# Kernel tuning notes

Hardware: AMD Instinct MI355X
Metric: run time of the kernel (lower is better)

The kernel has to match this reference:

```python
import jax, jax.numpy as jnp
import numpy as np

COMMITMENT_COST = 0.25


def setup_inputs() -> dict:
    key = jax.random.key(0)
    k1, k2 = jax.random.split(key)
    x = jax.random.normal(k1, (65536, 256), dtype=jnp.float32)
    codebook = jax.random.normal(k2, (1024, 256), dtype=jnp.float32)
    return {"x": x, "codebook": codebook}


def reference(x, codebook):
    # Flatten to [N, D] (already 2D here).
    flat = x.reshape(-1, codebook.shape[1])
    # Squared euclidean distances [N, K]; argmin matches torch.cdist argmin.
    x2 = jnp.sum(flat * flat, axis=1, keepdims=True)          # [N, 1]
    c2 = jnp.sum(codebook * codebook, axis=1)                  # [K]
    d2 = x2 - 2.0 * (flat @ codebook.T) + c2[None, :]          # [N, K]
    encoding_indices = jnp.argmin(d2, axis=1)                  # [N]
    quantized = codebook[encoding_indices]                     # [N, D]
    # VQ loss + commitment loss
    vq_loss = jnp.mean((jax.lax.stop_gradient(quantized) - flat) ** 2)
    commitment_loss = jnp.mean((quantized - jax.lax.stop_gradient(flat)) ** 2)
    quantization_loss = vq_loss + COMMITMENT_COST * commitment_loss
    # Straight-through estimator
    quantized_st = flat + jax.lax.stop_gradient(quantized - flat)
    quantized_st = quantized_st.reshape(x.shape)
    return quantized_st, quantization_loss, encoding_indices
```

## Files before the change

### kernel.cpp

```cpp
#include <hip/hip_runtime.h>

#define NROWS 65536
#define DDIM  256
#define KCODES 1024
#define MARGIN 0.05f
#define TIE_WINDOW 8.0e-5
#define FLAGCAP 8192

typedef __attribute__((ext_vector_type(8))) short bf16x8;
typedef __attribute__((ext_vector_type(4))) float f32x4;

union F4 { float4 v; float f[4]; };

__device__ __forceinline__ unsigned bf16rne(float f) {
    unsigned u = __float_as_uint(f);
    return (u + 0x7fffu + ((u >> 16) & 1u)) >> 16;
}
__device__ __forceinline__ float bf16tof(unsigned h) {
    return __uint_as_float(h << 16);
}

__global__ __launch_bounds__(64) void c2_kernel(const float* __restrict__ cb,
                                                float* __restrict__ c2f,
                                                double* __restrict__ c2d,
                                                int* __restrict__ cnt) {
    const int c = blockIdx.x, lane = threadIdx.x;
    if (c == 0 && lane == 0) cnt[0] = 0;
    F4 v; v.v = reinterpret_cast<const float4*>(cb + (size_t)c * DDIM)[lane];
    double s = (double)v.f[0] * v.f[0] + (double)v.f[1] * v.f[1]
             + (double)v.f[2] * v.f[2] + (double)v.f[3] * v.f[3];
    #pragma unroll
    for (int off = 32; off; off >>= 1) s += __shfl_xor(s, off);
    if (lane == 0) { c2d[c] = s; c2f[c] = (float)s; }
}

__global__ __launch_bounds__(256) void prep_frags(const float* __restrict__ cb,
                                                  unsigned short* __restrict__ fh,
                                                  unsigned short* __restrict__ fl) {
    int t = blockIdx.x * 256 + threadIdx.x;
    int j0   = (t & 1) * 4;
    int lane = (t >> 1) & 63;
    int ks   = (t >> 7) & 7;
    int ntg  = t >> 10;
    int c = ntg * 16 + (lane & 15);
    int k = ks * 32 + (lane >> 4) * 8 + j0;
    F4 v; v.v = *reinterpret_cast<const float4*>(cb + (size_t)c * DDIM + k);
    unsigned h0 = bf16rne(v.f[0]), h1 = bf16rne(v.f[1]),
             h2 = bf16rne(v.f[2]), h3 = bf16rne(v.f[3]);
    unsigned l0 = bf16rne(v.f[0] - bf16tof(h0)), l1 = bf16rne(v.f[1] - bf16tof(h1)),
             l2 = bf16rne(v.f[2] - bf16tof(h2)), l3 = bf16rne(v.f[3] - bf16tof(h3));
    unsigned* ph = reinterpret_cast<unsigned*>(fh + (size_t)t * 4);
    unsigned* pl = reinterpret_cast<unsigned*>(fl + (size_t)t * 4);
    ph[0] = h0 | (h1 << 16); ph[1] = h2 | (h3 << 16);
    pl[0] = l0 | (l1 << 16); pl[1] = l2 | (l3 << 16);
}

__global__ __launch_bounds__(1024) void vqmfma(const float* __restrict__ x,
                                               const unsigned short* __restrict__ fbh,
                                               const unsigned short* __restrict__ fbl,
                                               const float* __restrict__ c2f,
                                               float* __restrict__ out_idx,
                                               int* __restrict__ flaglist,
                                               int* __restrict__ cnt) {
    __shared__ bf16x8 lds_ah[2048];
    __shared__ bf16x8 lds_al[2048];
    __shared__ float  lds_c2[KCODES];
    __shared__ float  m_b1[512]; __shared__ float m_b2[512]; __shared__ int m_i1[512];

    const int tid  = threadIdx.x;
    const int w    = tid >> 6;
    const int lane = tid & 63;
    const int rh   = w >> 3;
    const int g    = w & 7;
    const int row0 = blockIdx.x * 64;

    lds_c2[tid] = c2f[tid];

    {
        const float4* gx = reinterpret_cast<const float4*>(x + (size_t)row0 * DDIM);
        unsigned* pah = reinterpret_cast<unsigned*>(lds_ah);
        unsigned* pal = reinterpret_cast<unsigned*>(lds_al);
        #pragma unroll
        for (int jj = 0; jj < 4; jj++) {
            int flat4 = jj * 1024 + tid;
            int r = flat4 >> 6;
            int k = (flat4 & 63) * 4;
            F4 v; v.v = gx[flat4];
            int rt = r >> 4, row = r & 15;
            int ks = k >> 5, gg = (k >> 3) & 3, j0 = k & 7;
            int laneS = gg * 16 + row;
            int u32i = ((((rt * 8 + ks) * 64 + laneS) * 8 + j0) >> 1);
            unsigned h0 = bf16rne(v.f[0]), h1 = bf16rne(v.f[1]),
                     h2 = bf16rne(v.f[2]), h3 = bf16rne(v.f[3]);
            pah[u32i]     = h0 | (h1 << 16);
            pah[u32i + 1] = h2 | (h3 << 16);
            unsigned l0 = bf16rne(v.f[0] - bf16tof(h0)), l1 = bf16rne(v.f[1] - bf16tof(h1)),
                     l2 = bf16rne(v.f[2] - bf16tof(h2)), l3 = bf16rne(v.f[3] - bf16tof(h3));
            pal[u32i]     = l0 | (l1 << 16);
            pal[u32i + 1] = l2 | (l3 << 16);
        }
    }
    __syncthreads();

    float bestv[8], secv[8]; int besti[8];
    #pragma unroll
    for (int e = 0; e < 8; e++) { bestv[e] = 1e30f; secv[e] = 1e30f; besti[e] = 0; }

    const bf16x8* Bh = reinterpret_cast<const bf16x8*>(fbh);
    const bf16x8* Bl = reinterpret_cast<const bf16x8*>(fbl);

    for (int cc = 0; cc < KCODES; cc += 256) {
        f32x4 acc[2][2];
        #pragma unroll
        for (int rt = 0; rt < 2; rt++)
            #pragma unroll
            for (int nt = 0; nt < 2; nt++) acc[rt][nt] = (f32x4){0.f, 0.f, 0.f, 0.f};

        const int ntg0 = (cc >> 4) + g * 2;
        const bf16x8* b0h = Bh + (size_t)(ntg0 * 8) * 64 + lane;
        const bf16x8* b0l = Bl + (size_t)(ntg0 * 8) * 64 + lane;
        const bf16x8* b1h = b0h + 8 * 64;
        const bf16x8* b1l = b0l + 8 * 64;
        const bf16x8* a0  = &lds_ah[(rh * 2) * 8 * 64 + lane];
        const bf16x8* a1  = a0 + 8 * 64;
        const bf16x8* a0l = &lds_al[(rh * 2) * 8 * 64 + lane];
        const bf16x8* a1l = a0l + 8 * 64;

        #pragma unroll
        for (int ks = 0; ks < 8; ks++) {
            bf16x8 ah0 = a0[ks * 64],  ah1 = a1[ks * 64];
            bf16x8 al0 = a0l[ks * 64], al1 = a1l[ks * 64];
            bf16x8 bh0 = b0h[ks * 64], bl0 = b0l[ks * 64];
            bf16x8 bh1 = b1h[ks * 64], bl1 = b1l[ks * 64];
            acc[0][0] = __builtin_amdgcn_mfma_f32_16x16x32_bf16(ah0, bh0, acc[0][0], 0, 0, 0);
            acc[1][0] = __builtin_amdgcn_mfma_f32_16x16x32_bf16(ah1, bh0, acc[1][0], 0, 0, 0);
            acc[0][1] = __builtin_amdgcn_mfma_f32_16x16x32_bf16(ah0, bh1, acc[0][1], 0, 0, 0);
            acc[1][1] = __builtin_amdgcn_mfma_f32_16x16x32_bf16(ah1, bh1, acc[1][1], 0, 0, 0);
            acc[0][0] = __builtin_amdgcn_mfma_f32_16x16x32_bf16(ah0, bl0, acc[0][0], 0, 0, 0);
            acc[1][0] = __builtin_amdgcn_mfma_f32_16x16x32_bf16(ah1, bl0, acc[1][0], 0, 0, 0);
            acc[0][1] = __builtin_amdgcn_mfma_f32_16x16x32_bf16(ah0, bl1, acc[0][1], 0, 0, 0);
            acc[1][1] = __builtin_amdgcn_mfma_f32_16x16x32_bf16(ah1, bl1, acc[1][1], 0, 0, 0);
            acc[0][0] = __builtin_amdgcn_mfma_f32_16x16x32_bf16(al0, bh0, acc[0][0], 0, 0, 0);
            acc[1][0] = __builtin_amdgcn_mfma_f32_16x16x32_bf16(al1, bh0, acc[1][0], 0, 0, 0);
            acc[0][1] = __builtin_amdgcn_mfma_f32_16x16x32_bf16(al0, bh1, acc[0][1], 0, 0, 0);
            acc[1][1] = __builtin_amdgcn_mfma_f32_16x16x32_bf16(al1, bh1, acc[1][1], 0, 0, 0);
        }
        #pragma unroll
        for (int nt = 0; nt < 2; nt++) {
            int c = cc + g * 32 + nt * 16 + (lane & 15);
            float c2v = lds_c2[c];
            #pragma unroll
            for (int rt = 0; rt < 2; rt++)
                #pragma unroll
                for (int reg = 0; reg < 4; reg++) {
                    float s = __fmaf_rn(-2.f, acc[rt][nt][reg], c2v);
                    int e = rt * 4 + reg;
                    if (s < bestv[e]) { secv[e] = bestv[e]; bestv[e] = s; besti[e] = c; }
                    else if (s < secv[e]) secv[e] = s;
                }
        }
    }

    #pragma unroll
    for (int e = 0; e < 8; e++) {
        float b1 = bestv[e]; int i1 = besti[e]; float b2 = secv[e];
        #pragma unroll
        for (int off = 8; off; off >>= 1) {
            float o1 = __shfl_xor(b1, off, 16);
            int   oi = __shfl_xor(i1, off, 16);
            float o2 = __shfl_xor(b2, off, 16);
            if (o1 < b1 || (o1 == b1 && oi < i1)) { b2 = fminf(b1, o2); b1 = o1; i1 = oi; }
            else                                  { b2 = fminf(o1, b2); }
        }
        if ((lane & 15) == 0) {
            int rt = e >> 2, reg = e & 3;
            int rib = rh * 32 + rt * 16 + (lane >> 4) * 4 + reg;
            m_b1[g * 64 + rib] = b1; m_i1[g * 64 + rib] = i1; m_b2[g * 64 + rib] = b2;
        }
    }
    __syncthreads();

    if (tid < 64) {
        float b1 = m_b1[tid]; int i1 = m_i1[tid]; float b2 = m_b2[tid];
        #pragma unroll
        for (int gg = 1; gg < 8; gg++) {
            float o1 = m_b1[gg * 64 + tid]; int oi = m_i1[gg * 64 + tid];
            float o2 = m_b2[gg * 64 + tid];
            if (o1 < b1 || (o1 == b1 && oi < i1)) { b2 = fminf(b1, o2); b1 = o1; i1 = oi; }
            else                                  { b2 = fminf(o1, b2); }
        }
        out_idx[row0 + tid] = (float)i1;
        if (b2 - b1 < MARGIN) {
            int slot = atomicAdd(cnt, 1);
            if (slot < FLAGCAP) flaglist[slot] = row0 + tid;
        }
    }
}

__global__ __launch_bounds__(256) void refine_kernel(const float* __restrict__ x,
                                                     const float* __restrict__ cb,
                                                     const double* __restrict__ c2d,
                                                     const int* __restrict__ flaglist,
                                                     const int* __restrict__ cnt,
                                                     float* __restrict__ out_idx) {
    __shared__ double xs[DDIM];
    __shared__ double redd[256];
    __shared__ int    redi[256];
    const int tid = threadIdx.x;
    const int n = min(cnt[0], FLAGCAP);

    for (int fi = blockIdx.x; fi < n; fi += gridDim.x) {
        const int row = flaglist[fi];
        const double xv = (double)x[(size_t)row * DDIM + tid];
        xs[tid] = xv;
        redd[tid] = xv * xv;
        __syncthreads();
        for (int off = 128; off; off >>= 1) {
            if (tid < off) redd[tid] += redd[tid + off];
            __syncthreads();
        }
        const double x2 = redd[0];
        __syncthreads();

        double d2v[4];
        #pragma unroll
        for (int j = 0; j < 4; j++) {
            const int c = tid + 256 * j;
            const float* cp = cb + (size_t)c * DDIM;
            double dot = 0.0;
            for (int d = 0; d < DDIM; d += 4) {
                F4 cv; cv.v = *reinterpret_cast<const float4*>(cp + d);
                dot += xs[d+0]*(double)cv.f[0] + xs[d+1]*(double)cv.f[1]
                     + xs[d+2]*(double)cv.f[2] + xs[d+3]*(double)cv.f[3];
            }
            d2v[j] = x2 - 2.0 * dot + c2d[c];
        }
        double mv = fmin(fmin(d2v[0], d2v[1]), fmin(d2v[2], d2v[3]));
        redd[tid] = mv;
        __syncthreads();
        for (int off = 128; off; off >>= 1) {
            if (tid < off) redd[tid] = fmin(redd[tid], redd[tid + off]);
            __syncthreads();
        }
        const double thr = redd[0] + TIE_WINDOW;
        __syncthreads();
        int ci = 0x7fffffff;
        #pragma unroll
        for (int j = 0; j < 4; j++)
            if (d2v[j] <= thr) ci = min(ci, tid + 256 * j);
        redi[tid] = ci;
        __syncthreads();
        for (int off = 128; off; off >>= 1) {
            if (tid < off) redi[tid] = min(redi[tid], redi[tid + off]);
            __syncthreads();
        }
        if (tid == 0) out_idx[row] = (float)redi[0];
        __syncthreads();
    }
}

__global__ __launch_bounds__(256) void gather_kernel(const float* __restrict__ x,
                                                     const float* __restrict__ cb,
                                                     const float* __restrict__ out_idx,
                                                     float* __restrict__ out_q,
                                                     float* __restrict__ partial) {
    __shared__ float wsum[4];
    const int tid = threadIdx.x;
    const int row = blockIdx.x * 32 + (tid >> 3);
    const int d0  = (tid & 7) * 32;
    const int bi  = (int)out_idx[row];
    const float4* gq = reinterpret_cast<const float4*>(cb + (size_t)bi * DDIM + d0);
    const float4* gx = reinterpret_cast<const float4*>(x + (size_t)row * DDIM + d0);
    float4* go = reinterpret_cast<float4*>(out_q + (size_t)row * DDIM + d0);
    float sq = 0.f;
    #pragma unroll
    for (int j = 0; j < 8; j++) {
        F4 q, xv; q.v = gq[j]; xv.v = gx[j];
        go[j] = q.v;
        #pragma unroll
        for (int t = 0; t < 4; t++) { float d = q.f[t] - xv.f[t]; sq += d * d; }
    }
    #pragma unroll
    for (int off = 32; off; off >>= 1) sq += __shfl_down(sq, off);
    if ((tid & 63) == 0) wsum[tid >> 6] = sq;
    __syncthreads();
    if (tid == 0) partial[blockIdx.x] = wsum[0] + wsum[1] + wsum[2] + wsum[3];
}

__global__ __launch_bounds__(256) void loss_kernel(const float* __restrict__ partial,
                                                   float* __restrict__ out_loss) {
    __shared__ float w[4];
    float s = 0.f;
    for (int j = threadIdx.x; j < 2048; j += 256) s += partial[j];
    #pragma unroll
    for (int off = 32; off; off >>= 1) s += __shfl_down(s, off);
    if ((threadIdx.x & 63) == 0) w[threadIdx.x >> 6] = s;
    __syncthreads();
    if (threadIdx.x == 0)
        out_loss[0] = 1.25f * (w[0] + w[1] + w[2] + w[3]) / 16777216.f;
}

extern "C" void kernel_launch(void* const* d_in, const int* in_sizes, int n_in,
                              void* d_out, int out_size, void* d_ws, size_t ws_size,
                              hipStream_t stream) {
    const float* x  = (const float*)d_in[0];
    const float* cb = (const float*)d_in[1];
    float* out      = (float*)d_out;
    float* out_q    = out;
    float* out_loss = out + 16777216;
    float* out_idx  = out + 16777217;

    unsigned short* fbh = (unsigned short*)d_out;
    unsigned short* fbl = fbh + 262144;

    char* wsp = (char*)d_ws;
    float*  ws_c2f     = (float*) (wsp +     0);
    double* ws_c2d     = (double*)(wsp +  4096);
    float*  ws_partial = (float*) (wsp + 12288);
    int*    ws_flag    = (int*)   (wsp + 20480);
    int*    ws_cnt     = (int*)   (wsp + 53248);

    c2_kernel<<<KCODES, 64, 0, stream>>>(cb, ws_c2f, ws_c2d, ws_cnt);
    prep_frags<<<256, 256, 0, stream>>>(cb, fbh, fbl);
    vqmfma<<<NROWS / 64, 1024, 0, stream>>>(x, fbh, fbl, ws_c2f,
                                            out_idx, ws_flag, ws_cnt);
    refine_kernel<<<256, 256, 0, stream>>>(x, cb, ws_c2d, ws_flag, ws_cnt, out_idx);
    gather_kernel<<<NROWS / 32, 256, 0, stream>>>(x, cb, out_idx, out_q, ws_partial);
    loss_kernel<<<1, 256, 0, stream>>>(ws_partial, out_loss);
}
```

Baseline: 264.4 us.

## Fuse codebook gather and per-row loss into the distance kernel

The distance kernel now also writes the selected codebook row to the output and records each row's squared error, computed as best distance plus x². This lets the separate gather pass, which re-read x and wrote the 64MB quantized output, be dropped. A new refine kernel rewrites the output row and its error in double precision for rows near a tie, and a single-block kernel sums the per-row errors. The fused path depends on a larger workspace and falls back to the old pipeline otherwise; the loss now rests on the expanded-distance identity, which may carry more rounding error.

```diff
diff --git a/kernel.cpp b/kernel.cpp
--- a/kernel.cpp
+++ b/kernel.cpp
@@ -56,16 +56,22 @@
 }
 
 __global__ __launch_bounds__(1024) void vqmfma(const float* __restrict__ x,
+                                               const float* __restrict__ cb,
                                                const unsigned short* __restrict__ fbh,
                                                const unsigned short* __restrict__ fbl,
                                                const float* __restrict__ c2f,
                                                float* __restrict__ out_idx,
                                                int* __restrict__ flaglist,
-                                               int* __restrict__ cnt) {
+                                               int* __restrict__ cnt,
+                                               float* __restrict__ out_q,
+                                               float* __restrict__ rowsq,
+                                               int fuse) {
     __shared__ bf16x8 lds_ah[2048];
     __shared__ bf16x8 lds_al[2048];
     __shared__ float  lds_c2[KCODES];
     __shared__ float  m_b1[512]; __shared__ float m_b2[512]; __shared__ int m_i1[512];
+    __shared__ float  x2s[64];
+    __shared__ int    sbest[64];
 
     const int tid  = threadIdx.x;
     const int w    = tid >> 6;
@@ -80,12 +86,14 @@
         const float4* gx = reinterpret_cast<const float4*>(x + (size_t)row0 * DDIM);
         unsigned* pah = reinterpret_cast<unsigned*>(lds_ah);
         unsigned* pal = reinterpret_cast<unsigned*>(lds_al);
+        float sq4[4];
         #pragma unroll
         for (int jj = 0; jj < 4; jj++) {
             int flat4 = jj * 1024 + tid;
             int r = flat4 >> 6;
             int k = (flat4 & 63) * 4;
             F4 v; v.v = gx[flat4];
+            sq4[jj] = v.f[0]*v.f[0] + v.f[1]*v.f[1] + v.f[2]*v.f[2] + v.f[3]*v.f[3];
             int rt = r >> 4, row = r & 15;
             int ks = k >> 5, gg = (k >> 3) & 3, j0 = k & 7;
             int laneS = gg * 16 + row;
@@ -98,6 +106,13 @@
                      l2 = bf16rne(v.f[2] - bf16tof(h2)), l3 = bf16rne(v.f[3] - bf16tof(h3));
             pal[u32i]     = l0 | (l1 << 16);
             pal[u32i + 1] = l2 | (l3 << 16);
+        }
+        #pragma unroll
+        for (int jj = 0; jj < 4; jj++) {
+            float s = sq4[jj];
+            #pragma unroll
+            for (int off = 32; off; off >>= 1) s += __shfl_xor(s, off);
+            if (lane == 0) x2s[jj * 16 + w] = s;
         }
     }
     __syncthreads();
@@ -190,10 +205,99 @@
             else                                  { b2 = fminf(o1, b2); }
         }
         out_idx[row0 + tid] = (float)i1;
+        sbest[tid] = i1;
+        if (fuse) rowsq[row0 + tid] = b1 + x2s[tid];
         if (b2 - b1 < MARGIN) {
             int slot = atomicAdd(cnt, 1);
             if (slot < FLAGCAP) flaglist[slot] = row0 + tid;
         }
+    }
+    if (fuse) {
+        __syncthreads();
+        int r  = tid >> 4;
+        int d0 = (tid & 15) * 16;
+        int bi = sbest[r];
+        const float4* gq = reinterpret_cast<const float4*>(cb + (size_t)bi * DDIM + d0);
+        float4* go = reinterpret_cast<float4*>(out_q + (size_t)(row0 + r) * DDIM + d0);
+        go[0] = gq[0]; go[1] = gq[1]; go[2] = gq[2]; go[3] = gq[3];
+    }
+}
+
+__global__ __launch_bounds__(256) void refine_f(const float* __restrict__ x,
+                                                const float* __restrict__ cb,
+                                                const double* __restrict__ c2d,
+                                                const int* __restrict__ flaglist,
+                                                const int* __restrict__ cnt,
+                                                float* __restrict__ out_idx,
+                                                float* __restrict__ out_q,
+                                                float* __restrict__ rowsq) {
+    __shared__ double xs[DDIM];
+    __shared__ double redd[256];
+    __shared__ int    redi[256];
+    const int tid = threadIdx.x;
+    const int n = min(cnt[0], FLAGCAP);
+
+    for (int fi = blockIdx.x; fi < n; fi += gridDim.x) {
+        const int row = flaglist[fi];
+        const double xv = (double)x[(size_t)row * DDIM + tid];
+        xs[tid] = xv;
+        redd[tid] = xv * xv;
+        __syncthreads();
+        for (int off = 128; off; off >>= 1) {
+            if (tid < off) redd[tid] += redd[tid + off];
+            __syncthreads();
+        }
+        const double x2 = redd[0];
+        __syncthreads();
+
+        double d2v[4];
+        #pragma unroll
+        for (int j = 0; j < 4; j++) {
+            const int c = tid + 256 * j;
+            const float* cp = cb + (size_t)c * DDIM;
+            double dot = 0.0;
+            for (int d = 0; d < DDIM; d += 4) {
+                F4 cv; cv.v = *reinterpret_cast<const float4*>(cp + d);
+                dot += xs[d+0]*(double)cv.f[0] + xs[d+1]*(double)cv.f[1]
+                     + xs[d+2]*(double)cv.f[2] + xs[d+3]*(double)cv.f[3];
+            }
+            d2v[j] = x2 - 2.0 * dot + c2d[c];
+        }
+        double mv = fmin(fmin(d2v[0], d2v[1]), fmin(d2v[2], d2v[3]));
+        redd[tid] = mv;
+        __syncthreads();
+        for (int off = 128; off; off >>= 1) {
+            if (tid < off) redd[tid] = fmin(redd[tid], redd[tid + off]);
+            __syncthreads();
+        }
+        const double thr = redd[0] + TIE_WINDOW;
+        __syncthreads();
+        int ci = 0x7fffffff;
+        #pragma unroll
+        for (int j = 0; j < 4; j++)
+            if (d2v[j] <= thr) ci = min(ci, tid + 256 * j);
+        redi[tid] = ci;
+        __syncthreads();
+        for (int off = 128; off; off >>= 1) {
+            if (tid < off) redi[tid] = min(redi[tid], redi[tid + off]);
+            __syncthreads();
+        }
+        const int widx = redi[0];
+        __syncthreads();
+        const float qn = cb[(size_t)widx * DDIM + tid];
+        out_q[(size_t)row * DDIM + tid] = qn;
+        const double dn = (double)qn - xv;
+        redd[tid] = dn * dn;
+        __syncthreads();
+        for (int off = 128; off; off >>= 1) {
+            if (tid < off) redd[tid] += redd[tid + off];
+            __syncthreads();
+        }
+        if (tid == 0) {
+            rowsq[row]   = (float)redd[0];
+            out_idx[row] = (float)widx;
+        }
+        __syncthreads();
     }
 }
 
@@ -208,7 +312,6 @@
     __shared__ int    redi[256];
     const int tid = threadIdx.x;
     const int n = min(cnt[0], FLAGCAP);
-
     for (int fi = blockIdx.x; fi < n; fi += gridDim.x) {
         const int row = flaglist[fi];
         const double xv = (double)x[(size_t)row * DDIM + tid];
@@ -221,7 +324,6 @@
         }
         const double x2 = redd[0];
         __syncthreads();
-
         double d2v[4];
         #pragma unroll
         for (int j = 0; j < 4; j++) {
@@ -287,6 +389,23 @@
     if (tid == 0) partial[blockIdx.x] = wsum[0] + wsum[1] + wsum[2] + wsum[3];
 }
 
+__global__ __launch_bounds__(1024) void loss_rowsq(const float* __restrict__ rowsq,
+                                                   float* __restrict__ out_loss) {
+    __shared__ float w[16];
+    float s = 0.f;
+    for (int j = threadIdx.x; j < NROWS; j += 1024) s += rowsq[j];
+    #pragma unroll
+    for (int off = 32; off; off >>= 1) s += __shfl_down(s, off);
+    if ((threadIdx.x & 63) == 0) w[threadIdx.x >> 6] = s;
+    __syncthreads();
+    if (threadIdx.x == 0) {
+        float tot = 0.f;
+        #pragma unroll
+        for (int i = 0; i < 16; i++) tot += w[i];
+        out_loss[0] = 1.25f * tot / 16777216.f;
+    }
+}
+
 __global__ __launch_bounds__(256) void loss_kernel(const float* __restrict__ partial,
                                                    float* __restrict__ out_loss) {
     __shared__ float w[4];
@@ -310,21 +429,36 @@
     float* out_loss = out + 16777216;
     float* out_idx  = out + 16777217;
 
-    unsigned short* fbh = (unsigned short*)d_out;
-    unsigned short* fbl = fbh + 262144;
-
     char* wsp = (char*)d_ws;
-    float*  ws_c2f     = (float*) (wsp +     0);
-    double* ws_c2d     = (double*)(wsp +  4096);
-    float*  ws_partial = (float*) (wsp + 12288);
-    int*    ws_flag    = (int*)   (wsp + 20480);
-    int*    ws_cnt     = (int*)   (wsp + 53248);
+    float*  ws_c2f     = (float*) (wsp +      0);
+    double* ws_c2d     = (double*)(wsp +   4096);
+    int*    ws_flag    = (int*)   (wsp +  12288);
+    int*    ws_cnt     = (int*)   (wsp +  45056);
+    float*  ws_rowsq   = (float*) (wsp +  45120);
+    float*  ws_partial = (float*) (wsp + 307264);
+    unsigned short* ws_fbh = (unsigned short*)(wsp + 315456);
+    unsigned short* ws_fbl = ws_fbh + 262144;
+    const size_t NEED = 1364032;
 
     c2_kernel<<<KCODES, 64, 0, stream>>>(cb, ws_c2f, ws_c2d, ws_cnt);
-    prep_frags<<<256, 256, 0, stream>>>(cb, fbh, fbl);
-    vqmfma<<<NROWS / 64, 1024, 0, stream>>>(x, fbh, fbl, ws_c2f,
-                                            out_idx, ws_flag, ws_cnt);
-    refine_kernel<<<256, 256, 0, stream>>>(x, cb, ws_c2d, ws_flag, ws_cnt, out_idx);
-    gather_kernel<<<NROWS / 32, 256, 0, stream>>>(x, cb, out_idx, out_q, ws_partial);
-    loss_kernel<<<1, 256, 0, stream>>>(ws_partial, out_loss);
-}
+
+    if (ws_size >= NEED) {
+        prep_frags<<<256, 256, 0, stream>>>(cb, ws_fbh, ws_fbl);
+        vqmfma<<<NROWS / 64, 1024, 0, stream>>>(x, cb, ws_fbh, ws_fbl, ws_c2f,
+                                                out_idx, ws_flag, ws_cnt,
+                                                out_q, ws_rowsq, 1);
+        refine_f<<<256, 256, 0, stream>>>(x, cb, ws_c2d, ws_flag, ws_cnt,
+                                          out_idx, out_q, ws_rowsq);
+        loss_rowsq<<<1, 1024, 0, stream>>>(ws_rowsq, out_loss);
+    } else {
+        unsigned short* fbh = (unsigned short*)d_out;
+        unsigned short* fbl = fbh + 262144;
+        prep_frags<<<256, 256, 0, stream>>>(cb, fbh, fbl);
+        vqmfma<<<NROWS / 64, 1024, 0, stream>>>(x, cb, fbh, fbl, ws_c2f,
+                                                out_idx, ws_flag, ws_cnt,
+                                                out_q, ws_rowsq, 0);
+        refine_kernel<<<256, 256, 0, stream>>>(x, cb, ws_c2d, ws_flag, ws_cnt, out_idx);
+        gather_kernel<<<NROWS / 32, 256, 0, stream>>>(x, cb, out_idx, out_q, ws_partial);
+        loss_kernel<<<1, 256, 0, stream>>>(ws_partial, out_loss);
+    }
+}
```

Result: slower. 270.6 us (+2.3%).
